# Optimization experiments

Hardware: AMD Instinct MI355X
Metric: run time of the kernel (lower is better)

## Reference

```python
import jax, jax.numpy as jnp
import numpy as np

HIDDEN = 768

def setup_inputs() -> dict:
    key = jax.random.key(0)
    k1, k2, k3 = jax.random.split(key, 3)
    x = jax.random.normal(k1, (8, 2048, HIDDEN), dtype=jnp.float32)
    # nn.Linear(hidden, 3*hidden): weight [3H, H], bias [3H]; torch init ~ U(-1/sqrt(H), 1/sqrt(H))
    bound = 1.0 / np.sqrt(HIDDEN)
    W = jax.random.uniform(k2, (3 * HIDDEN, HIDDEN), dtype=jnp.float32, minval=-bound, maxval=bound)
    b = jax.random.uniform(k3, (3 * HIDDEN,), dtype=jnp.float32, minval=-bound, maxval=bound)
    return {"x": x, "W": W, "b": b}

def reference(x, W, b):
    # qkv: [B, N, 3H]
    qkv = jnp.einsum('bnd,hd->bnh', x, W) + b
    q, k, v = jnp.split(qkv, 3, axis=-1)  # each [B, N, H]
    # NOTE: original module applies NO 1/sqrt(d) scaling — kept faithful.
    weights = jnp.einsum('bnd,bmd->bnm', q, k)          # [B, N, N]
    weights = jax.nn.softmax(weights, axis=-1)
    out = jnp.einsum('bnm,bmd->bnd', weights, v)        # [B, N, H]
    return out
```

## Files before the change

### kernel.cpp

```cpp
#include <hip/hip_runtime.h>


typedef short    s16x8 __attribute__((ext_vector_type(8)));
typedef _Float16 h16x8 __attribute__((ext_vector_type(8)));
typedef _Float16 h16x4 __attribute__((ext_vector_type(4)));
typedef float    f32x4 __attribute__((ext_vector_type(4)));

__device__ __forceinline__ unsigned short f2bf(float x) {
    unsigned u = __float_as_uint(x);
    u += 0x7fffu + ((u >> 16) & 1u);
    return (unsigned short)(u >> 16);
}
__device__ __forceinline__ float bf2f(unsigned short h) {
    return __uint_as_float(((unsigned)h) << 16);
}
__device__ __forceinline__ unsigned short f2h(float x) {
    _Float16 h = (_Float16)x;
    unsigned short u;
    __builtin_memcpy(&u, &h, 2);
    return u;
}
__device__ __forceinline__ h16x8 as_h(s16x8 v) {
    h16x8 r; __builtin_memcpy(&r, &v, 16); return r;
}

__device__ __forceinline__ void gld16(const void* g, void* l) {
    __builtin_amdgcn_global_load_lds(
        (const __attribute__((address_space(1))) unsigned int*)(unsigned long long)g,
        (__attribute__((address_space(3))) unsigned int*)(unsigned)(unsigned long long)l,
        16, 0, 0);
}

template<bool FP16>
__device__ __forceinline__ f32x4 mma(s16x8 a, s16x8 b, f32x4 c) {
    if constexpr (FP16)
        return __builtin_amdgcn_mfma_f32_16x16x32_f16(as_h(a), as_h(b), c, 0, 0, 0);
    else
        return __builtin_amdgcn_mfma_f32_16x16x32_bf16(a, b, c, 0, 0, 0);
}

template<int MODE, bool FP16, int SWZ>
__global__ __launch_bounds__(512, 2)
void gemm_mfma(const unsigned short* __restrict__ A, const unsigned short* __restrict__ B,
               const float* __restrict__ bias, const float* __restrict__ rvec,
               float* __restrict__ Cf, unsigned short* __restrict__ Ch,
               int K, int lda, int ldb, int ldc,
               long long sA, long long sB, long long sC, long long sR)
{
    __shared__ unsigned short As[3][8192];
    __shared__ unsigned short Bs[3][8192];

    int bx = blockIdx.x, by = blockIdx.y, bz = blockIdx.z;
    if (SWZ == 1) {
        const int l = bx + gridDim.x * (by + gridDim.y * bz);
        bz = l & 7;
        const int t = l >> 3;
        bx = t % gridDim.x;
        by = t / gridDim.x;
    } else if (SWZ == 2) {
        const int l = bx + gridDim.x * by;
        const int c = l & 7;
        const int t = l >> 3;
        const int rows = gridDim.y >> 3;
        bx = t % gridDim.x;
        by = c * rows + t / gridDim.x;
    }

    A += (long long)bz * sA;
    B += (long long)bz * sB;

    const long long m0 = (long long)by * 256;
    const long long n0 = (long long)bx * 256;

    const int tid  = threadIdx.x;
    const int wave = tid >> 6, lane = tid & 63;
    const int wr = wave >> 2, wc = wave & 3;
    const int ml = lane & 15;
    const int ku = (((lane >> 4) ^ ((ml >> 1) & 3)) * 8);
    const int srr = wave * 16 + (lane >> 2);
    const int skc = (((lane & 3) ^ ((lane >> 3) & 3)) * 8);

    const int aidx = (wr * 128 + ml) * 32 + ku;
    const int bidx = (wc * 64  + ml) * 32 + ku;

    const unsigned short* Abase = A + (m0 + srr) * (long long)lda + skc;
    const unsigned short* Bbase = B + (n0 + srr) * (long long)ldb + skc;
    const long long a128 = 128LL * lda, b128 = 128LL * ldb;

    auto stage_a = [&](int t, int buf) {
        const unsigned short* p = Abase + t * 32;
        gld16(p,        &As[buf][wave * 512]);
        gld16(p + a128, &As[buf][4096 + wave * 512]);
    };
    auto stage_b = [&](int t, int buf) {
        const unsigned short* p = Bbase + t * 32;
        gld16(p,        &Bs[buf][wave * 512]);
        gld16(p + b128, &Bs[buf][4096 + wave * 512]);
    };

    f32x4 acc[8][4];
#pragma unroll
    for (int i = 0; i < 8; ++i)
#pragma unroll
        for (int j = 0; j < 4; ++j) acc[i][j] = f32x4{0.f, 0.f, 0.f, 0.f};

    const int nt = K >> 5;

    stage_a(0, 0); stage_b(0, 0);
    stage_a(1, 1); stage_b(1, 1);
    asm volatile("s_waitcnt vmcnt(4)" ::: "memory");
    __builtin_amdgcn_s_barrier();
    __builtin_amdgcn_sched_barrier(0);

    int cur = 0;
    for (int t = 0; t < nt; ++t) {
        const unsigned short* as = &As[cur][0];
        const unsigned short* bs = &Bs[cur][0];
        const bool pf2 = (t + 2 < nt);

        if (pf2) {
            const int nb = (cur >= 1) ? cur - 1 : 2;
            stage_a(t + 2, nb); stage_b(t + 2, nb);
        }

        s16x8 a8[8], b4[4];
#pragma unroll
        for (int i = 0; i < 4; ++i) a8[i] = *(const s16x8*)&as[aidx + i * 512];
#pragma unroll
        for (int j = 0; j < 4; ++j) b4[j] = *(const s16x8*)&bs[bidx + j * 512];
#pragma unroll
        for (int i = 0; i < 4; ++i) a8[4 + i] = *(const s16x8*)&as[aidx + (i + 4) * 512];

        __builtin_amdgcn_s_setprio(1);
#pragma unroll
        for (int i = 0; i < 8; ++i)
#pragma unroll
            for (int j = 0; j < 4; ++j)
                acc[i][j] = mma<FP16>(a8[i], b4[j], acc[i][j]);
        __builtin_amdgcn_s_setprio(0);

        if (pf2)               { asm volatile("s_waitcnt vmcnt(4)" ::: "memory"); }
        else if (t + 1 < nt)   { asm volatile("s_waitcnt vmcnt(0)" ::: "memory"); }
        __builtin_amdgcn_s_barrier();
        __builtin_amdgcn_sched_barrier(0);
        cur = (cur == 2) ? 0 : cur + 1;
    }

    const int r0 = (lane >> 4) * 4;
    const long long rowbase = m0 + wr * 128 + r0;
    const long long colbase = n0 + wc * 64 + ml;
    if (MODE == 1 || MODE == 2) {
#pragma unroll
        for (int i = 0; i < 8; ++i) {
            const long long rowb = rowbase + i * 16;
#pragma unroll
            for (int j = 0; j < 4; ++j) {
                const long long col = colbase + j * 16;
                const float bj = bias[col];
#pragma unroll
                for (int q = 0; q < 4; ++q) {
                    const float vv = acc[i][j][q] + bj;
                    Ch[(rowb + q) * (long long)ldc + col] = (MODE == 1) ? f2h(vv) : f2bf(vv);
                }
            }
        }
    } else if (MODE == 3) {
        Ch += (long long)bz * sC;
#pragma unroll
        for (int i = 0; i < 8; ++i) {
            const long long rowb = rowbase + i * 16;
#pragma unroll
            for (int j = 0; j < 4; ++j) {
                const long long col = colbase + j * 16;
#pragma unroll
                for (int q = 0; q < 4; ++q)
                    Ch[(rowb + q) * (long long)ldc + col] = f2bf(__expf(acc[i][j][q]));
            }
        }
    } else {
        Cf += (long long)bz * sC;
        rvec += (long long)bz * sR;
#pragma unroll
        for (int i = 0; i < 8; ++i) {
            const long long rowb = rowbase + i * 16;
#pragma unroll
            for (int j = 0; j < 4; ++j) {
                const long long col = colbase + j * 16;
#pragma unroll
                for (int q = 0; q < 4; ++q)
                    Cf[(rowb + q) * (long long)ldc + col] = acc[i][j][q] * rvec[rowb + q];
            }
        }
    }
}

__global__ __launch_bounds__(256)
void cvt_f16_2(const float* __restrict__ a, long long na4,
               const float* __restrict__ b, long long nb4,
               unsigned short* __restrict__ oa, unsigned short* __restrict__ ob)
{
    const long long i = (long long)blockIdx.x * 256 + threadIdx.x;
    const float4* src;
    h16x4* dst;
    long long idx;
    if (i < na4)            { src = (const float4*)a; dst = (h16x4*)oa; idx = i; }
    else if (i < na4 + nb4) { src = (const float4*)b; dst = (h16x4*)ob; idx = i - na4; }
    else return;
    const float4 v = src[idx];
    h16x4 o;
    o.x = (_Float16)v.x; o.y = (_Float16)v.y;
    o.z = (_Float16)v.z; o.w = (_Float16)v.w;
    dst[idx] = o;
}

__global__ __launch_bounds__(256)
void transpose_v(const unsigned short* __restrict__ v, unsigned short* __restrict__ vt)
{
    __shared__ unsigned short t[32][33];
    const int b = blockIdx.z;
    const int n0 = blockIdx.x * 32, h0 = blockIdx.y * 32;
    const int tx = threadIdx.x, ty = threadIdx.y;
    const unsigned short* src = v + (long long)b * 2048 * 768;
#pragma unroll
    for (int q = 0; q < 4; ++q)
        t[ty + q * 8][tx] = src[(long long)(n0 + ty + q * 8) * 768 + h0 + tx];
    __syncthreads();
    unsigned short* dst = vt + ((long long)b * 768 + h0) * 2048 + n0;
#pragma unroll
    for (int q = 0; q < 4; ++q)
        dst[(long long)(ty + q * 8) * 2048 + tx] = t[tx][ty + q * 8];
}

__global__ __launch_bounds__(256)
void rowsum_recip(const unsigned short* __restrict__ E, float* __restrict__ r)
{
    const long long row = blockIdx.x;
    const int t = threadIdx.x, lane = t & 63, w = t >> 6;
    __shared__ float red[4];
    const uint4 v = ((const uint4*)(E + row * 2048))[t];
    float s = bf2f((unsigned short)(v.x & 0xffff)) + bf2f((unsigned short)(v.x >> 16))
            + bf2f((unsigned short)(v.y & 0xffff)) + bf2f((unsigned short)(v.y >> 16))
            + bf2f((unsigned short)(v.z & 0xffff)) + bf2f((unsigned short)(v.z >> 16))
            + bf2f((unsigned short)(v.w & 0xffff)) + bf2f((unsigned short)(v.w >> 16));
#pragma unroll
    for (int o = 32; o; o >>= 1) s += __shfl_xor(s, o);
    if (lane == 0) red[w] = s;
    __syncthreads();
    if (t == 0) r[row] = 1.f / ((red[0] + red[1]) + (red[2] + red[3]));
}

extern "C" void kernel_launch(void* const* d_in, const int* in_sizes, int n_in,
                              void* d_out, int out_size, void* d_ws, size_t ws_size,
                              hipStream_t stream)
{
    const float* x    = (const float*)d_in[0];
    const float* W    = (const float*)d_in[1];
    const float* bias = (const float*)d_in[2];
    float* out = (float*)d_out;

    char* ws = (char*)d_ws;
    unsigned short* xh = (unsigned short*)ws;
    unsigned short* Wh = (unsigned short*)(ws + 25165824LL);
    unsigned short* qk = (unsigned short*)(ws + 28704768LL);
    unsigned short* v  = (unsigned short*)(ws + 79036416LL);
    unsigned short* vt = (unsigned short*)(ws + 104202240LL);
    unsigned short* E  = (unsigned short*)(ws + 129368064LL);
    float*          r  = (float*)(ws + 196476928LL);

    cvt_f16_2<<<dim3(14016), dim3(256), 0, stream>>>(
        x, 3145728LL, W, 442368LL, xh, Wh);

    gemm_mfma<1, true, 2><<<dim3(6, 64, 1), dim3(512), 0, stream>>>(
        xh, Wh, bias, nullptr, nullptr, qk,
        768, 768, 768, 1536, 0, 0, 0, 0);

    gemm_mfma<2, true, 2><<<dim3(3, 64, 1), dim3(512), 0, stream>>>(
        xh, Wh + 1536LL * 768, bias + 1536, nullptr, nullptr, v,
        768, 768, 768, 768, 0, 0, 0, 0);

    transpose_v<<<dim3(64, 24, 8), dim3(32, 8), 0, stream>>>(v, vt);

    gemm_mfma<3, true, 1><<<dim3(8, 8, 8), dim3(512), 0, stream>>>(
        qk, qk + 768, nullptr, nullptr, nullptr, E,
        768, 1536, 1536, 2048,
        2048LL * 1536, 2048LL * 1536, 2048LL * 2048, 0);

    rowsum_recip<<<dim3(16384), dim3(256), 0, stream>>>(E, r);

    gemm_mfma<4, false, 1><<<dim3(3, 8, 8), dim3(512), 0, stream>>>(
        E, vt, nullptr, r, out, nullptr,
        2048, 2048, 2048, 768,
        2048LL * 2048, 768LL * 2048, 2048LL * 768, 2048);
}
```

Baseline: 319.4 us.

## Fuse QKV projections into one launch and fold softmax row sums into exp GEMM

Merges the separate QK and V projection GEMMs into one launch that routes each output tile to the fp16 QK buffer or the bf16 V buffer by column. The exp-score GEMM now sums each row in its epilogue and adds the partials into a zeroed row-sum buffer with atomics, so the separate row-sum kernel and its full re-read of the score matrix are gone. The final GEMM takes the reciprocal itself, and the exp GEMM uses a two-stage LDS pipeline instead of three. The trade-off is an extra memset, atomic contention, summation order that depends on timing, and shallower prefetch in the score GEMM.

Result: slower. 345.5 us (+8.2%).

```diff
diff --git a/kernel.cpp b/kernel.cpp
--- a/kernel.cpp
+++ b/kernel.cpp
@@ -39,16 +39,18 @@
         return __builtin_amdgcn_mfma_f32_16x16x32_bf16(a, b, c, 0, 0, 0);
 }
 
-template<int MODE, bool FP16, int SWZ>
+template<int MODE, bool FP16, int SWZ, int DEPTH>
 __global__ __launch_bounds__(512, 2)
 void gemm_mfma(const unsigned short* __restrict__ A, const unsigned short* __restrict__ B,
                const float* __restrict__ bias, const float* __restrict__ rvec,
+               float* __restrict__ rsum,
                float* __restrict__ Cf, unsigned short* __restrict__ Ch,
+               unsigned short* __restrict__ Ch2,
                int K, int lda, int ldb, int ldc,
                long long sA, long long sB, long long sC, long long sR)
 {
-    __shared__ unsigned short As[3][8192];
-    __shared__ unsigned short Bs[3][8192];
+    __shared__ unsigned short As[DEPTH][8192];
+    __shared__ unsigned short Bs[DEPTH][8192];
 
     int bx = blockIdx.x, by = blockIdx.y, bz = blockIdx.z;
     if (SWZ == 1) {
@@ -106,50 +108,87 @@
 
     const int nt = K >> 5;
 
-    stage_a(0, 0); stage_b(0, 0);
-    stage_a(1, 1); stage_b(1, 1);
-    asm volatile("s_waitcnt vmcnt(4)" ::: "memory");
-    __builtin_amdgcn_s_barrier();
-    __builtin_amdgcn_sched_barrier(0);
-
-    int cur = 0;
-    for (int t = 0; t < nt; ++t) {
-        const unsigned short* as = &As[cur][0];
-        const unsigned short* bs = &Bs[cur][0];
-        const bool pf2 = (t + 2 < nt);
-
-        if (pf2) {
-            const int nb = (cur >= 1) ? cur - 1 : 2;
-            stage_a(t + 2, nb); stage_b(t + 2, nb);
-        }
-
-        s16x8 a8[8], b4[4];
-#pragma unroll
-        for (int i = 0; i < 4; ++i) a8[i] = *(const s16x8*)&as[aidx + i * 512];
-#pragma unroll
-        for (int j = 0; j < 4; ++j) b4[j] = *(const s16x8*)&bs[bidx + j * 512];
-#pragma unroll
-        for (int i = 0; i < 4; ++i) a8[4 + i] = *(const s16x8*)&as[aidx + (i + 4) * 512];
-
-        __builtin_amdgcn_s_setprio(1);
-#pragma unroll
-        for (int i = 0; i < 8; ++i)
-#pragma unroll
-            for (int j = 0; j < 4; ++j)
-                acc[i][j] = mma<FP16>(a8[i], b4[j], acc[i][j]);
-        __builtin_amdgcn_s_setprio(0);
-
-        if (pf2)               { asm volatile("s_waitcnt vmcnt(4)" ::: "memory"); }
-        else if (t + 1 < nt)   { asm volatile("s_waitcnt vmcnt(0)" ::: "memory"); }
+    if constexpr (DEPTH == 2) {
+        stage_a(0, 0); stage_b(0, 0);
+        asm volatile("s_waitcnt vmcnt(0)" ::: "memory");
         __builtin_amdgcn_s_barrier();
         __builtin_amdgcn_sched_barrier(0);
-        cur = (cur == 2) ? 0 : cur + 1;
+
+        for (int t = 0; t < nt; ++t) {
+            const int cur = t & 1, nb = cur ^ 1;
+            const unsigned short* as = &As[cur][0];
+            const unsigned short* bs = &Bs[cur][0];
+            const bool pf = (t + 1 < nt);
+
+            if (pf) { stage_a(t + 1, nb); stage_b(t + 1, nb); }
+
+            s16x8 a8[8], b4[4];
+#pragma unroll
+            for (int i = 0; i < 4; ++i) a8[i] = *(const s16x8*)&as[aidx + i * 512];
+#pragma unroll
+            for (int j = 0; j < 4; ++j) b4[j] = *(const s16x8*)&bs[bidx + j * 512];
+#pragma unroll
+            for (int i = 0; i < 4; ++i) a8[4 + i] = *(const s16x8*)&as[aidx + (i + 4) * 512];
+
+            __builtin_amdgcn_s_setprio(1);
+#pragma unroll
+            for (int i = 0; i < 8; ++i)
+#pragma unroll
+                for (int j = 0; j < 4; ++j)
+                    acc[i][j] = mma<FP16>(a8[i], b4[j], acc[i][j]);
+            __builtin_amdgcn_s_setprio(0);
+
+            if (pf) { asm volatile("s_waitcnt vmcnt(0)" ::: "memory"); }
+            __builtin_amdgcn_s_barrier();
+            __builtin_amdgcn_sched_barrier(0);
+        }
+    } else {
+        stage_a(0, 0); stage_b(0, 0);
+        stage_a(1, 1); stage_b(1, 1);
+        asm volatile("s_waitcnt vmcnt(4)" ::: "memory");
+        __builtin_amdgcn_s_barrier();
+        __builtin_amdgcn_sched_barrier(0);
+
+        int cur = 0;
+        for (int t = 0; t < nt; ++t) {
+            const unsigned short* as = &As[cur][0];
+            const unsigned short* bs = &Bs[cur][0];
+            const bool pf2 = (t + 2 < nt);
+
+            if (pf2) {
+                const int nb = (cur >= 1) ? cur - 1 : 2;
+                stage_a(t + 2, nb); stage_b(t + 2, nb);
+            }
+
+            s16x8 a8[8], b4[4];
+#pragma unroll
+            for (int i = 0; i < 4; ++i) a8[i] = *(const s16x8*)&as[aidx + i * 512];
+#pragma unroll
+            for (int j = 0; j < 4; ++j) b4[j] = *(const s16x8*)&bs[bidx + j * 512];
+#pragma unroll
+            for (int i = 0; i < 4; ++i) a8[4 + i] = *(const s16x8*)&as[aidx + (i + 4) * 512];
+
+            __builtin_amdgcn_s_setprio(1);
+#pragma unroll
+            for (int i = 0; i < 8; ++i)
+#pragma unroll
+                for (int j = 0; j < 4; ++j)
+                    acc[i][j] = mma<FP16>(a8[i], b4[j], acc[i][j]);
+            __builtin_amdgcn_s_setprio(0);
+
+            if (pf2)               { asm volatile("s_waitcnt vmcnt(4)" ::: "memory"); }
+            else if (t + 1 < nt)   { asm volatile("s_waitcnt vmcnt(0)" ::: "memory"); }
+            __builtin_amdgcn_s_barrier();
+            __builtin_amdgcn_sched_barrier(0);
+            cur = (cur == 2) ? 0 : cur + 1;
+        }
     }
 
     const int r0 = (lane >> 4) * 4;
     const long long rowbase = m0 + wr * 128 + r0;
     const long long colbase = n0 + wc * 64 + ml;
-    if (MODE == 1 || MODE == 2) {
+    if (MODE == 5) {
+        const bool qkpart = (n0 < 1536);
 #pragma unroll
         for (int i = 0; i < 8; ++i) {
             const long long rowb = rowbase + i * 16;
@@ -160,21 +199,46 @@
 #pragma unroll
                 for (int q = 0; q < 4; ++q) {
                     const float vv = acc[i][j][q] + bj;
-                    Ch[(rowb + q) * (long long)ldc + col] = (MODE == 1) ? f2h(vv) : f2bf(vv);
+                    if (qkpart) Ch [(rowb + q) * 1536LL + col]          = f2h(vv);
+                    else        Ch2[(rowb + q) *  768LL + (col - 1536)] = f2bf(vv);
                 }
             }
         }
     } else if (MODE == 3) {
         Ch += (long long)bz * sC;
+        float* rs = rsum + (long long)bz * sR;
 #pragma unroll
         for (int i = 0; i < 8; ++i) {
             const long long rowb = rowbase + i * 16;
+            float srow0 = 0.f, srow1 = 0.f, srow2 = 0.f, srow3 = 0.f;
 #pragma unroll
             for (int j = 0; j < 4; ++j) {
                 const long long col = colbase + j * 16;
-#pragma unroll
-                for (int q = 0; q < 4; ++q)
-                    Ch[(rowb + q) * (long long)ldc + col] = f2bf(__expf(acc[i][j][q]));
+                {
+                    const unsigned short u0 = f2bf(__expf(acc[i][j][0]));
+                    const unsigned short u1 = f2bf(__expf(acc[i][j][1]));
+                    const unsigned short u2 = f2bf(__expf(acc[i][j][2]));
+                    const unsigned short u3 = f2bf(__expf(acc[i][j][3]));
+                    Ch[(rowb + 0) * (long long)ldc + col] = u0;
+                    Ch[(rowb + 1) * (long long)ldc + col] = u1;
+                    Ch[(rowb + 2) * (long long)ldc + col] = u2;
+                    Ch[(rowb + 3) * (long long)ldc + col] = u3;
+                    srow0 += bf2f(u0); srow1 += bf2f(u1);
+                    srow2 += bf2f(u2); srow3 += bf2f(u3);
+                }
+            }
+#pragma unroll
+            for (int o = 1; o < 16; o <<= 1) {
+                srow0 += __shfl_xor(srow0, o);
+                srow1 += __shfl_xor(srow1, o);
+                srow2 += __shfl_xor(srow2, o);
+                srow3 += __shfl_xor(srow3, o);
+            }
+            if (ml == 0) {
+                atomicAdd(&rs[rowb + 0], srow0);
+                atomicAdd(&rs[rowb + 1], srow1);
+                atomicAdd(&rs[rowb + 2], srow2);
+                atomicAdd(&rs[rowb + 3], srow3);
             }
         }
     } else {
@@ -183,12 +247,17 @@
 #pragma unroll
         for (int i = 0; i < 8; ++i) {
             const long long rowb = rowbase + i * 16;
+            float inv0 = 1.0f / rvec[rowb + 0];
+            float inv1 = 1.0f / rvec[rowb + 1];
+            float inv2 = 1.0f / rvec[rowb + 2];
+            float inv3 = 1.0f / rvec[rowb + 3];
 #pragma unroll
             for (int j = 0; j < 4; ++j) {
                 const long long col = colbase + j * 16;
-#pragma unroll
-                for (int q = 0; q < 4; ++q)
-                    Cf[(rowb + q) * (long long)ldc + col] = acc[i][j][q] * rvec[rowb + q];
+                Cf[(rowb + 0) * (long long)ldc + col] = acc[i][j][0] * inv0;
+                Cf[(rowb + 1) * (long long)ldc + col] = acc[i][j][1] * inv1;
+                Cf[(rowb + 2) * (long long)ldc + col] = acc[i][j][2] * inv2;
+                Cf[(rowb + 3) * (long long)ldc + col] = acc[i][j][3] * inv3;
             }
         }
     }
@@ -231,24 +300,6 @@
         dst[(long long)(ty + q * 8) * 2048 + tx] = t[tx][ty + q * 8];
 }
 
-__global__ __launch_bounds__(256)
-void rowsum_recip(const unsigned short* __restrict__ E, float* __restrict__ r)
-{
-    const long long row = blockIdx.x;
-    const int t = threadIdx.x, lane = t & 63, w = t >> 6;
-    __shared__ float red[4];
-    const uint4 v = ((const uint4*)(E + row * 2048))[t];
-    float s = bf2f((unsigned short)(v.x & 0xffff)) + bf2f((unsigned short)(v.x >> 16))
-            + bf2f((unsigned short)(v.y & 0xffff)) + bf2f((unsigned short)(v.y >> 16))
-            + bf2f((unsigned short)(v.z & 0xffff)) + bf2f((unsigned short)(v.z >> 16))
-            + bf2f((unsigned short)(v.w & 0xffff)) + bf2f((unsigned short)(v.w >> 16));
-#pragma unroll
-    for (int o = 32; o; o >>= 1) s += __shfl_xor(s, o);
-    if (lane == 0) red[w] = s;
-    __syncthreads();
-    if (t == 0) r[row] = 1.f / ((red[0] + red[1]) + (red[2] + red[3]));
-}
-
 extern "C" void kernel_launch(void* const* d_in, const int* in_sizes, int n_in,
                               void* d_out, int out_size, void* d_ws, size_t ws_size,
                               hipStream_t stream)
@@ -270,25 +321,21 @@
     cvt_f16_2<<<dim3(14016), dim3(256), 0, stream>>>(
         x, 3145728LL, W, 442368LL, xh, Wh);
 
-    gemm_mfma<1, true, 2><<<dim3(6, 64, 1), dim3(512), 0, stream>>>(
-        xh, Wh, bias, nullptr, nullptr, qk,
-        768, 768, 768, 1536, 0, 0, 0, 0);
-
-    gemm_mfma<2, true, 2><<<dim3(3, 64, 1), dim3(512), 0, stream>>>(
-        xh, Wh + 1536LL * 768, bias + 1536, nullptr, nullptr, v,
-        768, 768, 768, 768, 0, 0, 0, 0);
+    hipMemsetAsync(r, 0, 16384 * sizeof(float), stream);
+
+    gemm_mfma<5, true, 2, 3><<<dim3(9, 64, 1), dim3(512), 0, stream>>>(
+        xh, Wh, bias, nullptr, nullptr, nullptr, qk, v,
+        768, 768, 768, 0, 0, 0, 0, 0);
 
     transpose_v<<<dim3(64, 24, 8), dim3(32, 8), 0, stream>>>(v, vt);
 
-    gemm_mfma<3, true, 1><<<dim3(8, 8, 8), dim3(512), 0, stream>>>(
-        qk, qk + 768, nullptr, nullptr, nullptr, E,
+    gemm_mfma<3, true, 1, 2><<<dim3(8, 8, 8), dim3(512), 0, stream>>>(
+        qk, qk + 768, nullptr, nullptr, r, nullptr, E, nullptr,
         768, 1536, 1536, 2048,
-        2048LL * 1536, 2048LL * 1536, 2048LL * 2048, 0);
-
-    rowsum_recip<<<dim3(16384), dim3(256), 0, stream>>>(E, r);
-
-    gemm_mfma<4, false, 1><<<dim3(3, 8, 8), dim3(512), 0, stream>>>(
-        E, vt, nullptr, r, out, nullptr,
+        2048LL * 1536, 2048LL * 1536, 2048LL * 2048, 2048);
+
+    gemm_mfma<4, false, 1, 3><<<dim3(3, 8, 8), dim3(512), 0, stream>>>(
+        E, vt, nullptr, r, nullptr, out, nullptr, nullptr,
         2048, 2048, 2048, 768,
         2048LL * 2048, 768LL * 2048, 2048LL * 768, 2048);
 }
```

## Restructure GEMM mainloop into 8-phase ping-pong schedule with BK=64 tiles

Applied to the files above, without the earlier changes.

Replaces the triple-buffered BK=32 loop with double-buffered BK=64 tiles and a new XOR swizzle. Each K-tile pair is split into eight phases, each holding a quarter of the MFMAs, with partial LDS loads and global prefetches interleaved between barriers. The aim is finer-grained overlap of global-to-LDS staging, LDS reads and MFMA work, plus fewer iterations. It adds many more barriers and complex vmcnt accounting, which risks stalls or correctness problems if the counts are wrong. It also assumes K is a multiple of 128.

After: 324.6 us. About the same (+1.6%).

```diff
diff --git a/kernel.cpp b/kernel.cpp
--- a/kernel.cpp
+++ b/kernel.cpp
@@ -47,8 +47,8 @@
                int K, int lda, int ldb, int ldc,
                long long sA, long long sB, long long sC, long long sR)
 {
-    __shared__ unsigned short As[3][8192];
-    __shared__ unsigned short Bs[3][8192];
+    __shared__ unsigned short As[2][16384];
+    __shared__ unsigned short Bs[2][16384];
 
     int bx = blockIdx.x, by = blockIdx.y, bz = blockIdx.z;
     if (SWZ == 1) {
@@ -76,26 +76,50 @@
     const int wave = tid >> 6, lane = tid & 63;
     const int wr = wave >> 2, wc = wave & 3;
     const int ml = lane & 15;
-    const int ku = (((lane >> 4) ^ ((ml >> 1) & 3)) * 8);
-    const int srr = wave * 16 + (lane >> 2);
-    const int skc = (((lane & 3) ^ ((lane >> 3) & 3)) * 8);
-
-    const int aidx = (wr * 128 + ml) * 32 + ku;
-    const int bidx = (wc * 64  + ml) * 32 + ku;
-
-    const unsigned short* Abase = A + (m0 + srr) * (long long)lda + skc;
-    const unsigned short* Bbase = B + (n0 + srr) * (long long)ldb + skc;
-    const long long a128 = 128LL * lda, b128 = 128LL * ldb;
-
-    auto stage_a = [&](int t, int buf) {
-        const unsigned short* p = Abase + t * 32;
-        gld16(p,        &As[buf][wave * 512]);
-        gld16(p + a128, &As[buf][4096 + wave * 512]);
-    };
-    auto stage_b = [&](int t, int buf) {
-        const unsigned short* p = Bbase + t * 32;
-        gld16(p,        &Bs[buf][wave * 512]);
-        gld16(p + b128, &Bs[buf][4096 + wave * 512]);
+    const int ua0 = (((lane >> 4)    ) ^ (ml & 7)) * 8;
+    const int ua1 = (((lane >> 4) + 4) ^ (ml & 7)) * 8;
+    const int srow = wave * 8 + (lane >> 3);
+    const int skc  = ((lane & 7) ^ (lane >> 3)) * 8;
+    const int sc5 = srow >> 5, s31 = srow & 31;
+
+    const int aro = (wr * 64 + ml) * 64;
+    const int bro = (wc * 32 + ml) * 64;
+
+    const int ntile = K >> 6;
+    const int npair = ntile >> 1;
+
+    const unsigned short* Asrc = A + (m0 + srow) * (long long)lda + skc;
+    const unsigned short* Bsrc = B + (n0 + s31) * (long long)ldb + skc;
+
+    auto stA = [&](int kt, int buf, int h) {
+        if (kt >= ntile) return;
+#pragma unroll
+        for (int c = 0; c < 2; ++c)
+            gld16(Asrc + (long long)(h * 64 + c * 128) * lda + kt * 64,
+                  &As[buf][(h * 128 + c * 64 + wave * 8) * 64]);
+    };
+    auto stB = [&](int kt, int buf, int hB) {
+        if (kt >= ntile) return;
+#pragma unroll
+        for (int c = 0; c < 2; ++c)
+            gld16(Bsrc + (long long)((c * 2 + sc5) * 64 + hB * 32) * ldb + kt * 64,
+                  &Bs[buf][(hB * 128 + c * 64 + wave * 8) * 64]);
+    };
+
+    s16x8 af[4][2], bf0[2][2], bf1[2][2];
+    auto ldA = [&](const unsigned short* bp, int h) {
+#pragma unroll
+        for (int i = 0; i < 4; ++i) {
+            af[i][0] = *(const s16x8*)&bp[h * 8192 + aro + i * 1024 + ua0];
+            af[i][1] = *(const s16x8*)&bp[h * 8192 + aro + i * 1024 + ua1];
+        }
+    };
+    auto ldB = [&](const unsigned short* bp, int hB, s16x8 bf[2][2]) {
+#pragma unroll
+        for (int jj = 0; jj < 2; ++jj) {
+            bf[jj][0] = *(const s16x8*)&bp[hB * 8192 + bro + jj * 1024 + ua0];
+            bf[jj][1] = *(const s16x8*)&bp[hB * 8192 + bro + jj * 1024 + ua1];
+        }
     };
 
     f32x4 acc[8][4];
@@ -104,47 +128,79 @@
 #pragma unroll
         for (int j = 0; j < 4; ++j) acc[i][j] = f32x4{0.f, 0.f, 0.f, 0.f};
 
-    const int nt = K >> 5;
-
-    stage_a(0, 0); stage_b(0, 0);
-    stage_a(1, 1); stage_b(1, 1);
+    auto mfmaQ = [&](int ib, int jb, s16x8 bf[2][2]) {
+        __builtin_amdgcn_s_setprio(1);
+#pragma unroll
+        for (int s = 0; s < 2; ++s)
+#pragma unroll
+            for (int i = 0; i < 4; ++i)
+#pragma unroll
+                for (int jj = 0; jj < 2; ++jj)
+                    acc[ib + i][jb + jj] = mma<FP16>(af[i][s], bf[jj][s], acc[ib + i][jb + jj]);
+        __builtin_amdgcn_s_setprio(0);
+    };
+
+#define PH_SYNC  __builtin_amdgcn_s_barrier();                              \
+                 asm volatile("s_waitcnt lgkmcnt(0)" ::: "memory");          \
+                 __builtin_amdgcn_sched_barrier(0);
+#define PH_END   __builtin_amdgcn_s_barrier();                              \
+                 __builtin_amdgcn_sched_barrier(0);
+
+    stA(0, 0, 0); stB(0, 0, 0);
+    stB(0, 0, 1); stA(0, 0, 1);
     asm volatile("s_waitcnt vmcnt(4)" ::: "memory");
+    stA(1, 1, 0); stB(1, 1, 1); stA(1, 1, 1);
+    asm volatile("s_waitcnt vmcnt(6)" ::: "memory");
     __builtin_amdgcn_s_barrier();
     __builtin_amdgcn_sched_barrier(0);
 
-    int cur = 0;
-    for (int t = 0; t < nt; ++t) {
-        const unsigned short* as = &As[cur][0];
-        const unsigned short* bs = &Bs[cur][0];
-        const bool pf2 = (t + 2 < nt);
-
-        if (pf2) {
-            const int nb = (cur >= 1) ? cur - 1 : 2;
-            stage_a(t + 2, nb); stage_b(t + 2, nb);
-        }
-
-        s16x8 a8[8], b4[4];
-#pragma unroll
-        for (int i = 0; i < 4; ++i) a8[i] = *(const s16x8*)&as[aidx + i * 512];
-#pragma unroll
-        for (int j = 0; j < 4; ++j) b4[j] = *(const s16x8*)&bs[bidx + j * 512];
-#pragma unroll
-        for (int i = 0; i < 4; ++i) a8[4 + i] = *(const s16x8*)&as[aidx + (i + 4) * 512];
-
-        __builtin_amdgcn_s_setprio(1);
-#pragma unroll
-        for (int i = 0; i < 8; ++i)
-#pragma unroll
-            for (int j = 0; j < 4; ++j)
-                acc[i][j] = mma<FP16>(a8[i], b4[j], acc[i][j]);
-        __builtin_amdgcn_s_setprio(0);
-
-        if (pf2)               { asm volatile("s_waitcnt vmcnt(4)" ::: "memory"); }
-        else if (t + 1 < nt)   { asm volatile("s_waitcnt vmcnt(0)" ::: "memory"); }
-        __builtin_amdgcn_s_barrier();
-        __builtin_amdgcn_sched_barrier(0);
-        cur = (cur == 2) ? 0 : cur + 1;
+    for (int it = 0; it < npair; ++it) {
+        const int ta = 2 * it, tb = 2 * it + 1;
+        const bool last = (it == npair - 1);
+        const unsigned short* a0 = &As[0][0];
+        const unsigned short* b0 = &Bs[0][0];
+        const unsigned short* a1 = &As[1][0];
+        const unsigned short* b1 = &Bs[1][0];
+
+        ldA(a0, 0); ldB(b0, 0, bf0);
+        stB(tb, 1, 0);
+        PH_SYNC; mfmaQ(0, 0, bf0); PH_END;
+
+        ldB(b0, 1, bf1);
+        stA(ta + 2, 0, 0);
+        PH_SYNC; mfmaQ(0, 2, bf1); PH_END;
+
+        ldA(a0, 1);
+        stB(ta + 2, 0, 1);
+        PH_SYNC; mfmaQ(4, 2, bf1); PH_END;
+
+        ldB(b0, 0, bf0);
+        stA(ta + 2, 0, 1);
+        PH_SYNC; mfmaQ(4, 0, bf0);
+        if (!last) { asm volatile("s_waitcnt vmcnt(6)" ::: "memory"); }
+        else       { asm volatile("s_waitcnt vmcnt(0)" ::: "memory"); }
+        PH_END;
+
+        ldA(a1, 0); ldB(b1, 0, bf0);
+        stB(ta + 2, 0, 0);
+        PH_SYNC; mfmaQ(0, 0, bf0); PH_END;
+
+        ldB(b1, 1, bf1);
+        stA(tb + 2, 1, 0);
+        PH_SYNC; mfmaQ(0, 2, bf1); PH_END;
+
+        ldA(a1, 1);
+        stB(tb + 2, 1, 1);
+        PH_SYNC; mfmaQ(4, 2, bf1); PH_END;
+
+        ldB(b1, 0, bf0);
+        stA(tb + 2, 1, 1);
+        PH_SYNC; mfmaQ(4, 0, bf0);
+        if (it + 1 < npair) { asm volatile("s_waitcnt vmcnt(6)" ::: "memory"); }
+        PH_END;
     }
+#undef PH_SYNC
+#undef PH_END
 
     const int r0 = (lane >> 4) * 4;
     const long long rowbase = m0 + wr * 128 + r0;
```
